# Performance work log

Measured on AMD Instinct MI355X. Metric: run time of the kernel, lower is better.

The kernel has to match this reference:

```python
import jax, jax.numpy as jnp
import numpy as np

D_IN = 2048
D_OUT = 2048
NUM_HEADS = 16
HEAD_DIM = D_OUT // NUM_HEADS
CONTEXT_LENGTH = 4096
THETA_BASE = 10000.0


def _rope_tables(seq_len):
    half = HEAD_DIM // 2
    inv_freq = 1.0 / (THETA_BASE ** (jnp.arange(half, dtype=jnp.float32) / half))
    positions = jnp.arange(seq_len, dtype=jnp.float32)
    angles = positions[:, None] * inv_freq[None, :]          # [S, half]
    angles = jnp.concatenate([angles, angles], axis=-1)      # [S, HEAD_DIM]
    return jnp.cos(angles), jnp.sin(angles)


def _apply_rope(x, cos, sin):
    # x: [B, H, S, D]
    half = x.shape[-1] // 2
    x1, x2 = x[..., :half], x[..., half:]
    rotated = jnp.concatenate([-x2, x1], axis=-1)
    return x * cos[None, None, :, :] + rotated * sin[None, None, :, :]


def setup_inputs() -> dict:
    key = jax.random.key(0)
    ks = jax.random.split(key, 5)
    x = jax.random.normal(ks[0], (1, 4096, D_IN), dtype=jnp.float32)
    scale_in = 1.0 / np.sqrt(D_IN)
    scale_out = 1.0 / np.sqrt(D_OUT)
    w_q = jax.random.normal(ks[1], (D_OUT, D_IN), dtype=jnp.float32) * scale_in
    w_k = jax.random.normal(ks[2], (D_OUT, D_IN), dtype=jnp.float32) * scale_in
    w_v = jax.random.normal(ks[3], (D_OUT, D_IN), dtype=jnp.float32) * scale_in
    w_o = jax.random.normal(ks[4], (D_IN, D_OUT), dtype=jnp.float32) * scale_out
    return {"x": x, "w_q": w_q, "w_k": w_k, "w_v": w_v, "w_o": w_o}


def reference(x, w_q, w_k, w_v, w_o):
    b, s, _ = x.shape
    cos, sin = _rope_tables(s)

    def split_heads(t):  # [B,S,D_OUT] -> [B,H,S,HEAD_DIM]
        return t.reshape(b, s, NUM_HEADS, HEAD_DIM).transpose(0, 2, 1, 3)

    q = split_heads(jnp.einsum('bsd,od->bso', x, w_q))
    k = split_heads(jnp.einsum('bsd,od->bso', x, w_k))
    v = split_heads(jnp.einsum('bsd,od->bso', x, w_v))

    q = _apply_rope(q, cos, sin)
    k = _apply_rope(k, cos, sin)

    scores = jnp.einsum('bhqd,bhkd->bhqk', q, k) / jnp.sqrt(jnp.float32(HEAD_DIM))
    causal = jnp.tril(jnp.ones((s, s), dtype=bool))
    scores = jnp.where(causal[None, None, :, :], scores, -jnp.inf)
    attn = jax.nn.softmax(scores, axis=-1)

    ctx = jnp.einsum('bhqk,bhkd->bhqd', attn, v)  # [B,H,S,HEAD_DIM]
    ctx = ctx.transpose(0, 2, 1, 3).reshape(b, s, D_OUT)
    return jnp.einsum('bso,do->bsd', ctx, w_o)
```

## Files before the change

### kernel.cpp

```cpp
#include <hip/hip_runtime.h>
#include <hip/hip_bf16.h>
#include <stdint.h>

#define SEQ 4096
#define DM 2048
#define NH 16
#define HD 128

typedef __attribute__((ext_vector_type(4)))  float f32x4;
typedef __attribute__((ext_vector_type(16))) float f32x16;
typedef __attribute__((ext_vector_type(8)))  short bf16x8;
typedef __attribute__((ext_vector_type(4)))  float float4_t;
typedef __attribute__((ext_vector_type(4)))  short s16x4;
typedef __attribute__((ext_vector_type(2)))  int   i32x2;
typedef __attribute__((ext_vector_type(2)))  unsigned u32x2;

__device__ __forceinline__ short f2bf(float f) {
  union { float f; unsigned u; } c; c.f = f;
  unsigned u = c.u;
  u += 0x7FFFu + ((u >> 16) & 1u);
  return (short)(u >> 16);
}

__device__ __forceinline__ int cvtpk(float lo, float hi) {
  int r;
  asm("v_cvt_pk_bf16_f32 %0, %1, %2" : "=v"(r) : "v"(lo), "v"(hi));
  return r;
}

__device__ __forceinline__ float exp2r(float x) {
  return __builtin_amdgcn_exp2f(x);
}

__device__ __forceinline__ void async16(const void* g, void* l) {
  __builtin_amdgcn_global_load_lds((const __attribute__((address_space(1))) void*)g,
                                   (__attribute__((address_space(3))) void*)l, 16, 0, 0);
}

__global__ __launch_bounds__(256) void rope_tables_kernel(float2* __restrict__ tab) {
  int idx = blockIdx.x * 256 + threadIdx.x;
  int s = idx >> 6, j = idx & 63;
  float invf = expf(-(float)j * (9.210340371976184f / 64.0f));
  float ang = (float)s * invf;
  tab[idx] = make_float2(cosf(ang), sinf(ang));
}

__global__ __launch_bounds__(256) void f32_to_bf16_kernel(const float* __restrict__ in,
                                                          short* __restrict__ out, int n4) {
  int stride = gridDim.x * 256;
  for (int i = blockIdx.x * 256 + threadIdx.x; i < n4; i += stride) {
    float4_t v = ((const float4_t*)in)[i];
    s16x4 r;
    #pragma unroll
    for (int u = 0; u < 4; u++) r[u] = f2bf(v[u]);
    ((s16x4*)out)[i] = r;
  }
}

template<int MODE>
__global__ __launch_bounds__(512) void gemm8p_kernel(
    const short* __restrict__ A, const short* __restrict__ B,
    void* __restrict__ Cp, const float2* __restrict__ tab) {
  constexpr int MM = SEQ, NN = DM, K = DM;
  __shared__ __align__(16) char LB[147456];
  const int t = threadIdx.x, lane = t & 63, w = t >> 6;
  const int wm = w >> 1, wn = w & 1;
  const size_t Mbase = (size_t)blockIdx.x * 256;
  const size_t Nbase = (size_t)blockIdx.y * 128;
  const int nt = K / 64;

  auto stageA = [&](int kt, int half) {
    const int buf = kt % 3, k0 = kt * 64;
    #pragma unroll
    for (int it = 0; it < 2; it++) {
      const int ob = half * 16384 + it * 8192 + w * 1024;
      const int o = ob + lane * 16;
      const int row = o >> 7;
      const int col = (o & 127) ^ ((row & 7) << 4);
      async16((const char*)A + ((Mbase + row) * (size_t)K + k0) * 2 + col,
              LB + buf * 32768 + ob);
    }
  };
  auto stageB = [&](int kt) {
    const int buf = kt % 3, k0 = kt * 64;
    #pragma unroll
    for (int it = 0; it < 2; it++) {
      const int ob = it * 8192 + w * 1024;
      const int o = ob + lane * 16;
      const int row = o >> 7;
      const int col = (o & 127) ^ ((row & 7) << 4);
      async16((const char*)B + ((Nbase + row) * (size_t)K + k0) * 2 + col,
              LB + 98304 + buf * 16384 + ob);
    }
  };

  f32x4 acc[4][4] = {};

  stageA(0, 0); stageA(0, 1); stageB(0);
  stageA(1, 0); stageA(1, 1); stageB(1);
  asm volatile("s_waitcnt vmcnt(6)" ::: "memory");
  __builtin_amdgcn_s_barrier();

  for (int kt = 0; kt < nt; kt++) {
    const char* AsB = LB + (kt % 3) * 32768;
    const char* BsB = LB + 98304 + (kt % 3) * 16384;
    const bool pre = (kt + 2 < nt);
    bf16x8 a[2][4], b[2][2];

    #pragma unroll
    for (int ks = 0; ks < 2; ks++)
      #pragma unroll
      for (int m = 0; m < 4; m++) {
        int row = wm * 64 + m * 16 + (lane & 15);
        a[ks][m] = *(const bf16x8*)(AsB + row * 128
                    + ((ks * 64 + (lane >> 4) * 16) ^ ((row & 7) << 4)));
      }
    #pragma unroll
    for (int ks = 0; ks < 2; ks++)
      #pragma unroll
      for (int n = 0; n < 2; n++) {
        int row = n * 32 + wn * 16 + (lane & 15);
        b[ks][n] = *(const bf16x8*)(BsB + row * 128
                    + ((ks * 64 + (lane >> 4) * 16) ^ ((row & 7) << 4)));
      }
    if (pre) { stageA(kt + 2, 0); stageA(kt + 2, 1); }
    __builtin_amdgcn_s_barrier();
    asm volatile("s_waitcnt lgkmcnt(0)" ::: "memory");
    __builtin_amdgcn_sched_barrier(0);
    __builtin_amdgcn_s_setprio(1);
    #pragma unroll
    for (int ks = 0; ks < 2; ks++)
      #pragma unroll
      for (int m = 0; m < 4; m++)
        #pragma unroll
        for (int n = 0; n < 2; n++)
          acc[m][n] = __builtin_amdgcn_mfma_f32_16x16x32_bf16(
              a[ks][m], b[ks][n], acc[m][n], 0, 0, 0);
    __builtin_amdgcn_s_setprio(0);
    __builtin_amdgcn_s_barrier();

    #pragma unroll
    for (int ks = 0; ks < 2; ks++)
      #pragma unroll
      for (int n = 0; n < 2; n++) {
        int row = (n + 2) * 32 + wn * 16 + (lane & 15);
        b[ks][n] = *(const bf16x8*)(BsB + row * 128
                    + ((ks * 64 + (lane >> 4) * 16) ^ ((row & 7) << 4)));
      }
    if (pre) stageB(kt + 2);
    if (pre) asm volatile("s_waitcnt vmcnt(6)" ::: "memory");
    else     asm volatile("s_waitcnt vmcnt(0)" ::: "memory");
    __builtin_amdgcn_s_barrier();
    asm volatile("s_waitcnt lgkmcnt(0)" ::: "memory");
    __builtin_amdgcn_sched_barrier(0);
    __builtin_amdgcn_s_setprio(1);
    #pragma unroll
    for (int ks = 0; ks < 2; ks++)
      #pragma unroll
      for (int m = 0; m < 4; m++)
        #pragma unroll
        for (int n = 0; n < 2; n++)
          acc[m][n + 2] = __builtin_amdgcn_mfma_f32_16x16x32_bf16(
              a[ks][m], b[ks][n], acc[m][n + 2], 0, 0, 0);
    __builtin_amdgcn_s_setprio(0);
    __builtin_amdgcn_s_barrier();
  }

  if (MODE == 1 || MODE == 2) {
    const float SC = (MODE == 1) ? 0.12751746f : 1.0f;
    #pragma unroll
    for (int m = 0; m < 4; m++)
      #pragma unroll
      for (int n = 0; n < 2; n++)
        #pragma unroll
        for (int j = 0; j < 4; j++) {
          int row = (int)Mbase + wm * 64 + m * 16 + (lane >> 4) * 4 + j;
          int dj = n * 32 + wn * 16 + (lane & 15);
          float2 cs = tab[row * 64 + dj];
          float cc = cs.x * SC, ss = cs.y * SC;
          float r1 = acc[m][n][j], r2 = acc[m][n + 2][j];
          short* C = (short*)Cp;
          C[(size_t)row * NN + Nbase + dj]      = f2bf(r1 * cc - r2 * ss);
          C[(size_t)row * NN + Nbase + dj + 64] = f2bf(r2 * cc + r1 * ss);
        }
  } else {
    #pragma unroll
    for (int m = 0; m < 4; m++)
      #pragma unroll
      for (int n = 0; n < 4; n++)
        #pragma unroll
        for (int j = 0; j < 4; j++) {
          size_t row = Mbase + wm * 64 + m * 16 + (lane >> 4) * 4 + j;
          size_t col = Nbase + n * 32 + wn * 16 + (lane & 15);
          float v = acc[m][n][j];
          if (MODE == 0) ((float*)Cp)[row * NN + col] = v;
          else           ((short*)Cp)[col * (size_t)MM + row] = f2bf(v);
        }
  }
}

__global__ __launch_bounds__(512) void flash_attn9_kernel(
    const short* __restrict__ Q, const short* __restrict__ K,
    const short* __restrict__ VT, short* __restrict__ O) {
  __shared__ __align__(16) char LB[65536];
  const int t = threadIdx.x, lane = t & 63, w = t >> 6;
  const int hi = lane >> 5, c31 = lane & 31;
  const int s = w & 3, v = w >> 2;
  const int id = blockIdx.x;
  const int h  = (id & 7) * 2 + ((id >> 3) & 1);
  const int pr = (id >> 4) & 15;
  const int qt = (id < 256) ? pr : (31 - pr);

  auto stage = [&](int kt, int buf) {
    #pragma unroll
    for (int it = 0; it < 2; it++) {
      const int ob = it * 8192 + w * 1024;
      const int o  = ob + lane * 16;
      const int row = o >> 8;
      const int xs = (o & 255) ^ ((row & 15) << 4);
      { const size_t src = ((size_t)(kt * 64 + row) * DM + h * HD) * 2 + xs;
        async16((const char*)K + src, LB + buf * 16384 + ob); }
      { const int d = 2 * row + (xs >> 7);
        const size_t src = ((size_t)(h * HD + d) * SEQ + (size_t)kt * 64) * 2
                         + (size_t)(xs & 127);
        async16((const char*)VT + src, LB + 32768 + buf * 16384 + ob); }
    }
  };

  const int q0 = qt * 128;
  const int nt = 2 * (qt + 1);
  const int qrow = q0 + s * 32 + c31;

  stage(0, 0);

  bf16x8 qf[8];
  #pragma unroll
  for (int ss = 0; ss < 8; ss++)
    qf[ss] = *(const bf16x8*)(Q + (size_t)qrow * DM + h * HD + ss * 16 + hi * 8);

  f32x16 oacc[4] = {};
  float m = -3.0e38f, l = 0.f;

  __syncthreads();

  for (int kt = 0; kt < nt; kt++) {
    const int buf = kt & 1;
    if (kt + 1 < nt) stage(kt + 1, buf ^ 1);

    if (kt * 64 + v * 32 <= q0 + s * 32 + 31) {
      const char* KsB = LB + buf * 16384;
      const char* VsB = LB + 32768 + buf * 16384;

      f32x16 sacc = {};
      __builtin_amdgcn_s_setprio(1);
      #pragma unroll
      for (int ss = 0; ss < 8; ss++) {
        int row = v * 32 + c31;
        bf16x8 kf = *(const bf16x8*)(KsB + row * 256
                                     + ((ss * 32 + hi * 16) ^ ((row & 15) << 4)));
        sacc = __builtin_amdgcn_mfma_f32_32x32x16_bf16(kf, qf[ss], sacc, 0, 0, 0);
      }
      __builtin_amdgcn_s_setprio(0);

      float t0[8];
      #pragma unroll
      for (int r = 0; r < 8; r++) t0[r] = fmaxf(sacc[r], sacc[r + 8]);
      #pragma unroll
      for (int d = 4; d > 0; d >>= 1)
        #pragma unroll
        for (int r = 0; r < 4; r++) if (r < d) t0[r] = fmaxf(t0[r], t0[r + d]);
      float mx = t0[0];
      i32x2 mm = __builtin_amdgcn_permlane32_swap(__float_as_int(mx), __float_as_int(mx),
                                                  false, false);
      mx = fmaxf(__int_as_float(mm.x), __int_as_float(mm.y));

      if (__any(mx > m + 11.5416f)) {
        float mn = fmaxf(m, mx);
        float al = exp2r(m - mn);
        m = mn; l *= al;
        #pragma unroll
        for (int g = 0; g < 4; g++)
          #pragma unroll
          for (int r = 0; r < 16; r++) oacc[g][r] *= al;
      }

      const int rel = qrow - kt * 64 - v * 32;
      const bool maskT = (kt * 64 + v * 32 + 31) > (q0 + s * 32);
      #pragma unroll
      for (int r = 0; r < 16; r++) {
        float e = exp2r(sacc[r] - m);
        if (maskT) {
          int kl = (r & 3) + 8 * (r >> 2) + 4 * hi;
          e = (kl > rel) ? 0.f : e;
        }
        sacc[r] = e;
      }

      float s0[8];
      #pragma unroll
      for (int r = 0; r < 8; r++) s0[r] = sacc[r] + sacc[r + 8];
      #pragma unroll
      for (int d = 4; d > 0; d >>= 1)
        #pragma unroll
        for (int r = 0; r < 4; r++) if (r < d) s0[r] = s0[r] + s0[r + d];
      l += s0[0];

      bf16x8 pa[2];
      #pragma unroll
      for (int sg = 0; sg < 2; sg++) {
        int q0a = cvtpk(sacc[8 * sg + 0], sacc[8 * sg + 1]);
        int q1a = cvtpk(sacc[8 * sg + 2], sacc[8 * sg + 3]);
        int q0b = cvtpk(sacc[8 * sg + 4], sacc[8 * sg + 5]);
        int q1b = cvtpk(sacc[8 * sg + 6], sacc[8 * sg + 7]);
        i32x2 r0 = __builtin_amdgcn_permlane32_swap(q0a, q0b, false, false);
        i32x2 r1 = __builtin_amdgcn_permlane32_swap(q1a, q1b, false, false);
        union { int d[4]; bf16x8 vv; } u;
        u.d[0] = r0.x; u.d[1] = r1.x; u.d[2] = r0.y; u.d[3] = r1.y;
        pa[sg] = u.vv;
      }

      __builtin_amdgcn_s_setprio(1);
      #pragma unroll
      for (int ks = 0; ks < 2; ks++)
        #pragma unroll
        for (int g = 0; g < 4; g++) {
          int d = g * 32 + c31;
          int row = d >> 1;
          int x = (d & 1) * 128 + v * 64 + ks * 32 + hi * 16;
          bf16x8 vf = *(const bf16x8*)(VsB + row * 256 + (x ^ ((row & 15) << 4)));
          oacc[g] = __builtin_amdgcn_mfma_f32_32x32x16_bf16(vf, pa[ks], oacc[g], 0, 0, 0);
        }
      __builtin_amdgcn_s_setprio(0);
    }
    __syncthreads();
  }

  i32x2 lr = __builtin_amdgcn_permlane32_swap(__float_as_int(l), __float_as_int(l),
                                              false, false);
  l = __int_as_float(lr.x) + __int_as_float(lr.y);

  #pragma unroll
  for (int round = 0; round < 2; round++) {
    const int reg = s & 1;
    const bool active = (s >> 1) == round;
    if (active && v == 1) {
      float* Op = (float*)(LB + reg * 16384);
      #pragma unroll
      for (int g = 0; g < 4; g++)
        #pragma unroll
        for (int rr = 0; rr < 16; rr++) {
          int d = g * 32 + (rr & 3) + 8 * (rr >> 2) + 4 * hi;
          Op[d * 32 + c31] = oacc[g][rr];
        }
      if (hi == 0) {
        float* mm2 = (float*)(LB + 32768 + reg * 256) + c31 * 2;
        mm2[0] = m; mm2[1] = l;
      }
    }
    __syncthreads();
    if (active && v == 0) {
      const float* mm2 = (const float*)(LB + 32768 + reg * 256) + c31 * 2;
      float lB = mm2[1];
      float mB = (lB > 0.f) ? mm2[0] : -3.0e38f;
      float ms = fmaxf(m, mB);
      float aA = exp2r(m - ms), aB = exp2r(mB - ms);
      float linv = 1.0f / (l * aA + lB * aB);
      float sA = aA * linv, sB = aB * linv;
      const float* Op = (const float*)(LB + reg * 16384);
      #pragma unroll
      for (int g = 0; g < 4; g++)
        #pragma unroll
        for (int tt = 0; tt < 4; tt++) {
          float o[4];
          #pragma unroll
          for (int e = 0; e < 4; e++) {
            int d = g * 32 + e + 8 * tt + 4 * hi;
            o[e] = oacc[g][4 * tt + e] * sA + Op[d * 32 + c31] * sB;
          }
          u32x2 pk;
          pk.x = (unsigned)cvtpk(o[0], o[1]);
          pk.y = (unsigned)cvtpk(o[2], o[3]);
          *(u32x2*)(O + (size_t)qrow * DM + h * HD + g * 32 + tt * 8 + hi * 4) = pk;
        }
    }
    __syncthreads();
  }
}

extern "C" void kernel_launch(void* const* d_in, const int* in_sizes, int n_in,
                              void* d_out, int out_size, void* d_ws, size_t ws_size,
                              hipStream_t stream) {
  const float* x  = (const float*)d_in[0];
  const float* wq = (const float*)d_in[1];
  const float* wk = (const float*)d_in[2];
  const float* wv = (const float*)d_in[3];
  const float* wo = (const float*)d_in[4];
  float* out = (float*)d_out;

  const size_t SQDMs = (size_t)SEQ * DM;
  short* Qb   = (short*)d_ws;
  short* Kb   = Qb + SQDMs;
  short* VTb  = Kb + SQDMs;
  short* Cb   = VTb + SQDMs;
  short* xbf  = Cb + SQDMs;
  short* wbuf = xbf + SQDMs;
  float2* tab = (float2*)(wbuf + (size_t)DM * DM);

  rope_tables_kernel<<<SEQ * 64 / 256, 256, 0, stream>>>(tab);
  f32_to_bf16_kernel<<<2048, 256, 0, stream>>>(x, xbf, (int)(SQDMs / 4));

  dim3 g8(SEQ / 256, DM / 128);
  f32_to_bf16_kernel<<<2048, 256, 0, stream>>>(wq, wbuf, DM * DM / 4);
  gemm8p_kernel<1><<<g8, 512, 0, stream>>>(xbf, wbuf, Qb, tab);
  f32_to_bf16_kernel<<<2048, 256, 0, stream>>>(wk, wbuf, DM * DM / 4);
  gemm8p_kernel<2><<<g8, 512, 0, stream>>>(xbf, wbuf, Kb, tab);
  f32_to_bf16_kernel<<<2048, 256, 0, stream>>>(wv, wbuf, DM * DM / 4);
  gemm8p_kernel<3><<<g8, 512, 0, stream>>>(xbf, wbuf, VTb, nullptr);

  flash_attn9_kernel<<<512, 512, 0, stream>>>(Qb, Kb, VTb, Cb);

  f32_to_bf16_kernel<<<2048, 256, 0, stream>>>(wo, wbuf, DM * DM / 4);
  gemm8p_kernel<0><<<g8, 512, 0, stream>>>(Cb, wbuf, out, nullptr);
}
```

Before: 281.1 us.

## Fuse Q/K/V projection GEMMs and weight conversions into single launches

Converts all three projection weights to bf16 in one kernel and runs the Q, K and V projection GEMMs as one launch with a 48-wide grid, where each block's y-index selects which output and epilogue it uses (RoPE for Q/K, transposed store for V). This cuts kernel launches and raises the number of concurrent blocks per GEMM, which improves CU occupancy. It needs a larger workspace, and falls back to the split path when the workspace is too small. The output projection gets its own specialised kernel.

```diff
diff --git a/kernel.cpp b/kernel.cpp
--- a/kernel.cpp
+++ b/kernel.cpp
@@ -57,16 +57,36 @@
   }
 }
 
-template<int MODE>
-__global__ __launch_bounds__(512) void gemm8p_kernel(
+__global__ __launch_bounds__(256) void w3_to_bf16_kernel(
+    const float* __restrict__ wq, const float* __restrict__ wk,
+    const float* __restrict__ wv, short* __restrict__ out) {
+  const int n4w = DM * DM / 4;
+  int stride = gridDim.x * 256;
+  for (int i = blockIdx.x * 256 + threadIdx.x; i < 3 * n4w; i += stride) {
+    int j = i >> 20;
+    int loc = i & (n4w - 1);
+    const float* src = (j == 0) ? wq : (j == 1) ? wk : wv;
+    float4_t v = ((const float4_t*)src)[loc];
+    s16x4 r;
+    #pragma unroll
+    for (int u = 0; u < 4; u++) r[u] = f2bf(v[u]);
+    ((s16x4*)out)[i] = r;
+  }
+}
+
+__global__ __launch_bounds__(512) void gemm_qkv_kernel(
     const short* __restrict__ A, const short* __restrict__ B,
-    void* __restrict__ Cp, const float2* __restrict__ tab) {
-  constexpr int MM = SEQ, NN = DM, K = DM;
+    short* __restrict__ Qout, short* __restrict__ Kout, short* __restrict__ VTout,
+    const float2* __restrict__ tab, int region) {
+  constexpr int NN = DM, K = DM, MM = SEQ;
   __shared__ __align__(16) char LB[147456];
   const int t = threadIdx.x, lane = t & 63, w = t >> 6;
   const int wm = w >> 1, wn = w & 1;
   const size_t Mbase = (size_t)blockIdx.x * 256;
-  const size_t Nbase = (size_t)blockIdx.y * 128;
+  const int ry  = (region < 0) ? (blockIdx.y >> 4) : region;
+  const int nyl = (region < 0) ? (blockIdx.y & 15) : blockIdx.y;
+  const size_t Bbase = (size_t)blockIdx.y * 128;
+  const size_t Nbase = (size_t)nyl * 128;
   const int nt = K / 64;
 
   auto stageA = [&](int kt, int half) {
@@ -89,7 +109,7 @@
       const int o = ob + lane * 16;
       const int row = o >> 7;
       const int col = (o & 127) ^ ((row & 7) << 4);
-      async16((const char*)B + ((Nbase + row) * (size_t)K + k0) * 2 + col,
+      async16((const char*)B + ((Bbase + row) * (size_t)K + k0) * 2 + col,
               LB + 98304 + buf * 16384 + ob);
     }
   };
@@ -166,8 +186,9 @@
     __builtin_amdgcn_s_barrier();
   }
 
-  if (MODE == 1 || MODE == 2) {
-    const float SC = (MODE == 1) ? 0.12751746f : 1.0f;
+  if (ry < 2) {
+    const float SC = (ry == 0) ? 0.12751746f : 1.0f;
+    short* C = (ry == 0) ? Qout : Kout;
     #pragma unroll
     for (int m = 0; m < 4; m++)
       #pragma unroll
@@ -179,7 +200,6 @@
           float2 cs = tab[row * 64 + dj];
           float cc = cs.x * SC, ss = cs.y * SC;
           float r1 = acc[m][n][j], r2 = acc[m][n + 2][j];
-          short* C = (short*)Cp;
           C[(size_t)row * NN + Nbase + dj]      = f2bf(r1 * cc - r2 * ss);
           C[(size_t)row * NN + Nbase + dj + 64] = f2bf(r2 * cc + r1 * ss);
         }
@@ -192,11 +212,129 @@
         for (int j = 0; j < 4; j++) {
           size_t row = Mbase + wm * 64 + m * 16 + (lane >> 4) * 4 + j;
           size_t col = Nbase + n * 32 + wn * 16 + (lane & 15);
-          float v = acc[m][n][j];
-          if (MODE == 0) ((float*)Cp)[row * NN + col] = v;
-          else           ((short*)Cp)[col * (size_t)MM + row] = f2bf(v);
+          VTout[col * (size_t)MM + row] = f2bf(acc[m][n][j]);
         }
   }
+}
+
+__global__ __launch_bounds__(512) void gemm_out_kernel(
+    const short* __restrict__ A, const short* __restrict__ B,
+    float* __restrict__ Cp) {
+  constexpr int NN = DM, K = DM;
+  __shared__ __align__(16) char LB[147456];
+  const int t = threadIdx.x, lane = t & 63, w = t >> 6;
+  const int wm = w >> 1, wn = w & 1;
+  const size_t Mbase = (size_t)blockIdx.x * 256;
+  const size_t Nbase = (size_t)blockIdx.y * 128;
+  const int nt = K / 64;
+
+  auto stageA = [&](int kt, int half) {
+    const int buf = kt % 3, k0 = kt * 64;
+    #pragma unroll
+    for (int it = 0; it < 2; it++) {
+      const int ob = half * 16384 + it * 8192 + w * 1024;
+      const int o = ob + lane * 16;
+      const int row = o >> 7;
+      const int col = (o & 127) ^ ((row & 7) << 4);
+      async16((const char*)A + ((Mbase + row) * (size_t)K + k0) * 2 + col,
+              LB + buf * 32768 + ob);
+    }
+  };
+  auto stageB = [&](int kt) {
+    const int buf = kt % 3, k0 = kt * 64;
+    #pragma unroll
+    for (int it = 0; it < 2; it++) {
+      const int ob = it * 8192 + w * 1024;
+      const int o = ob + lane * 16;
+      const int row = o >> 7;
+      const int col = (o & 127) ^ ((row & 7) << 4);
+      async16((const char*)B + ((Nbase + row) * (size_t)K + k0) * 2 + col,
+              LB + 98304 + buf * 16384 + ob);
+    }
+  };
+
+  f32x4 acc[4][4] = {};
+
+  stageA(0, 0); stageA(0, 1); stageB(0);
+  stageA(1, 0); stageA(1, 1); stageB(1);
+  asm volatile("s_waitcnt vmcnt(6)" ::: "memory");
+  __builtin_amdgcn_s_barrier();
+
+  for (int kt = 0; kt < nt; kt++) {
+    const char* AsB = LB + (kt % 3) * 32768;
+    const char* BsB = LB + 98304 + (kt % 3) * 16384;
+    const bool pre = (kt + 2 < nt);
+    bf16x8 a[2][4], b[2][2];
+
+    #pragma unroll
+    for (int ks = 0; ks < 2; ks++)
+      #pragma unroll
+      for (int m = 0; m < 4; m++) {
+        int row = wm * 64 + m * 16 + (lane & 15);
+        a[ks][m] = *(const bf16x8*)(AsB + row * 128
+                    + ((ks * 64 + (lane >> 4) * 16) ^ ((row & 7) << 4)));
+      }
+    #pragma unroll
+    for (int ks = 0; ks < 2; ks++)
+      #pragma unroll
+      for (int n = 0; n < 2; n++) {
+        int row = n * 32 + wn * 16 + (lane & 15);
+        b[ks][n] = *(const bf16x8*)(BsB + row * 128
+                    + ((ks * 64 + (lane >> 4) * 16) ^ ((row & 7) << 4)));
+      }
+    if (pre) { stageA(kt + 2, 0); stageA(kt + 2, 1); }
+    __builtin_amdgcn_s_barrier();
+    asm volatile("s_waitcnt lgkmcnt(0)" ::: "memory");
+    __builtin_amdgcn_sched_barrier(0);
+    __builtin_amdgcn_s_setprio(1);
+    #pragma unroll
+    for (int ks = 0; ks < 2; ks++)
+      #pragma unroll
+      for (int m = 0; m < 4; m++)
+        #pragma unroll
+        for (int n = 0; n < 2; n++)
+          acc[m][n] = __builtin_amdgcn_mfma_f32_16x16x32_bf16(
+              a[ks][m], b[ks][n], acc[m][n], 0, 0, 0);
+    __builtin_amdgcn_s_setprio(0);
+    __builtin_amdgcn_s_barrier();
+
+    #pragma unroll
+    for (int ks = 0; ks < 2; ks++)
+      #pragma unroll
+      for (int n = 0; n < 2; n++) {
+        int row = (n + 2) * 32 + wn * 16 + (lane & 15);
+        b[ks][n] = *(const bf16x8*)(BsB + row * 128
+                    + ((ks * 64 + (lane >> 4) * 16) ^ ((row & 7) << 4)));
+      }
+    if (pre) stageB(kt + 2);
+    if (pre) asm volatile("s_waitcnt vmcnt(6)" ::: "memory");
+    else     asm volatile("s_waitcnt vmcnt(0)" ::: "memory");
+    __builtin_amdgcn_s_barrier();
+    asm volatile("s_waitcnt lgkmcnt(0)" ::: "memory");
+    __builtin_amdgcn_sched_barrier(0);
+    __builtin_amdgcn_s_setprio(1);
+    #pragma unroll
+    for (int ks = 0; ks < 2; ks++)
+      #pragma unroll
+      for (int m = 0; m < 4; m++)
+        #pragma unroll
+        for (int n = 0; n < 2; n++)
+          acc[m][n + 2] = __builtin_amdgcn_mfma_f32_16x16x32_bf16(
+              a[ks][m], b[ks][n], acc[m][n + 2], 0, 0, 0);
+    __builtin_amdgcn_s_setprio(0);
+    __builtin_amdgcn_s_barrier();
+  }
+
+  #pragma unroll
+  for (int m = 0; m < 4; m++)
+    #pragma unroll
+    for (int n = 0; n < 4; n++)
+      #pragma unroll
+      for (int j = 0; j < 4; j++) {
+        size_t row = Mbase + wm * 64 + m * 16 + (lane >> 4) * 4 + j;
+        size_t col = Nbase + n * 32 + wn * 16 + (lane & 15);
+        Cp[row * NN + col] = acc[m][n][j];
+      }
 }
 
 __global__ __launch_bounds__(512) void flash_attn9_kernel(
@@ -404,21 +542,31 @@
   short* Cb   = VTb + SQDMs;
   short* xbf  = Cb + SQDMs;
   short* wbuf = xbf + SQDMs;
-  float2* tab = (float2*)(wbuf + (size_t)DM * DM);
+
+  const bool fused = ws_size >= (size_t)107 * 1024 * 1024;
+  float2* tab = (float2*)(wbuf + (fused ? (size_t)3 * DM * DM : (size_t)DM * DM));
 
   rope_tables_kernel<<<SEQ * 64 / 256, 256, 0, stream>>>(tab);
   f32_to_bf16_kernel<<<2048, 256, 0, stream>>>(x, xbf, (int)(SQDMs / 4));
 
-  dim3 g8(SEQ / 256, DM / 128);
-  f32_to_bf16_kernel<<<2048, 256, 0, stream>>>(wq, wbuf, DM * DM / 4);
-  gemm8p_kernel<1><<<g8, 512, 0, stream>>>(xbf, wbuf, Qb, tab);
-  f32_to_bf16_kernel<<<2048, 256, 0, stream>>>(wk, wbuf, DM * DM / 4);
-  gemm8p_kernel<2><<<g8, 512, 0, stream>>>(xbf, wbuf, Kb, tab);
-  f32_to_bf16_kernel<<<2048, 256, 0, stream>>>(wv, wbuf, DM * DM / 4);
-  gemm8p_kernel<3><<<g8, 512, 0, stream>>>(xbf, wbuf, VTb, nullptr);
+  if (fused) {
+    w3_to_bf16_kernel<<<2048, 256, 0, stream>>>(wq, wk, wv, wbuf);
+    gemm_qkv_kernel<<<dim3(SEQ / 256, 48), 512, 0, stream>>>(
+        xbf, wbuf, Qb, Kb, VTb, tab, -1);
+  } else {
+    f32_to_bf16_kernel<<<2048, 256, 0, stream>>>(wq, wbuf, DM * DM / 4);
+    gemm_qkv_kernel<<<dim3(SEQ / 256, 16), 512, 0, stream>>>(
+        xbf, wbuf, Qb, Kb, VTb, tab, 0);
+    f32_to_bf16_kernel<<<2048, 256, 0, stream>>>(wk, wbuf, DM * DM / 4);
+    gemm_qkv_kernel<<<dim3(SEQ / 256, 16), 512, 0, stream>>>(
+        xbf, wbuf, Qb, Kb, VTb, tab, 1);
+    f32_to_bf16_kernel<<<2048, 256, 0, stream>>>(wv, wbuf, DM * DM / 4);
+    gemm_qkv_kernel<<<dim3(SEQ / 256, 16), 512, 0, stream>>>(
+        xbf, wbuf, Qb, Kb, VTb, tab, 2);
+  }
 
   flash_attn9_kernel<<<512, 512, 0, stream>>>(Qb, Kb, VTb, Cb);
 
   f32_to_bf16_kernel<<<2048, 256, 0, stream>>>(wo, wbuf, DM * DM / 4);
-  gemm8p_kernel<0><<<g8, 512, 0, stream>>>(Cb, wbuf, out, nullptr);
-}
+  gemm_out_kernel<<<dim3(SEQ / 256, DM / 128), 512, 0, stream>>>(Cb, wbuf, out);
+}
```

Result: faster. 275.2 us (-2.1%).
